# Kernel tuning notes

Measured on AMD Instinct MI355X. Metric: run time of the kernel, lower is better.

Reference implementation:

```python
import jax, jax.numpy as jnp
import numpy as np

B, S, H, D = 4, 128, 32, 128
T = 2048  # max_seq_len (cache length)
START_POS = 1024


def setup_inputs() -> dict:
    key = jax.random.key(0)
    ks = jax.random.split(key, 5)
    q = jax.random.normal(ks[0], (B, S, H, D), dtype=jnp.float32)
    k = jax.random.normal(ks[1], (B, S, H, D), dtype=jnp.float32)
    v = jax.random.normal(ks[2], (B, S, H, D), dtype=jnp.float32)
    k_cache = jax.random.normal(ks[3], (B, T, H, D), dtype=jnp.float32)
    v_cache = jax.random.normal(ks[4], (B, T, H, D), dtype=jnp.float32)
    return {"q": q, "k": k, "v": v, "k_cache": k_cache, "v_cache": v_cache,
            "input_pos": START_POS, "seq_len": S}


def reference(q, k, v, k_cache, v_cache, input_pos, seq_len):
    # Fused KV-cache append + causal SDPA (llama.sdpa_with_kv_cache semantics).
    # q/k/v: [B, S, H, D]; caches: [B, T, H, D]; input_pos = write offset.
    start = input_pos
    kc = jax.lax.dynamic_update_slice(k_cache, k, (0, start, 0, 0))
    vc = jax.lax.dynamic_update_slice(v_cache, v, (0, start, 0, 0))

    scale = 1.0 / jnp.sqrt(jnp.asarray(q.shape[-1], q.dtype))
    # scores: [B, H, S, T]
    scores = jnp.einsum('bshd,bthd->bhst', q, kc) * scale

    # causal mask relative to absolute positions: query i (global start+i)
    # attends to cache positions j <= start + i
    qpos = start + jnp.arange(seq_len)            # [S]
    kpos = jnp.arange(kc.shape[1])                # [T]
    mask = kpos[None, :] <= qpos[:, None]         # [S, T]
    neg = jnp.asarray(jnp.finfo(scores.dtype).min, scores.dtype)
    scores = jnp.where(mask[None, None], scores, neg)

    attn = jax.nn.softmax(scores, axis=-1)        # dropout = 0.0 (inference)
    out = jnp.einsum('bhst,bthd->bshd', attn, vc)  # [B, S, H, D]
    bsz = q.shape[0]
    return out.reshape(bsz, seq_len, -1)          # [B, S, H*D]
```

## Files before the change

kernel.cpp:

```cpp
#include <hip/hip_runtime.h>
#include <hip/hip_bf16.h>


typedef short bf16x8 __attribute__((ext_vector_type(8)));
typedef float f32x4  __attribute__((ext_vector_type(4)));

constexpr int B = 4, S = 128, H = 32, D = 128, T = 2048;
constexpr int QBLK = 64, KVBLK = 64;
constexpr int NS = 4;
constexpr float SCALE = 0.08838834764831845f;
constexpr float MNEG = -1e30f;

__device__ __forceinline__ short f2bf(float f) {
    return (short)__bfloat16_as_ushort(__float2bfloat16(f));
}
__device__ __forceinline__ unsigned pack_bf2(float a, float b) {
    return (unsigned)(unsigned short)__bfloat16_as_ushort(__float2bfloat16(a))
         | ((unsigned)__bfloat16_as_ushort(__float2bfloat16(b)) << 16);
}

__device__ __forceinline__ int kswz(int row, int cb) { return row * 256 + (cb ^ ((row & 7) << 4)); }
__device__ __forceinline__ int vswz(int row, int cb) { return 16384 + row * 128 + (cb ^ ((row & 7) << 4)); }

template<int MODE>
__global__ __launch_bounds__(256, 4) void sdpa_kernel(
    const float* __restrict__ qg, const float* __restrict__ kin,
    const float* __restrict__ vin, const float* __restrict__ kc,
    const float* __restrict__ vc, const int* __restrict__ ip,
    float* __restrict__ out, float* __restrict__ wsO, float2* __restrict__ wsML)
{
    __shared__ __align__(16) char smem[32768];

    const int start = ip[0];
    const int bh = blockIdx.x;
    const int b  = bh >> 5;
    const int h  = bh & 31;
    const int q0 = blockIdx.y * QBLK;
    const int z  = (MODE == 1) ? blockIdx.z : 0;
    const int t  = threadIdx.x;
    const int w  = t >> 6;
    const int l  = t & 63;
    const int l16 = l & 15;
    const int lg  = l >> 4;
    const int qi  = q0 + w * 16 + l16;

    const float* qp = qg + (((size_t)b * S + qi) * H + h) * D;
    bf16x8 qfrag[4];
    #pragma unroll
    for (int ks = 0; ks < 4; ++ks) {
        const float* p = qp + ks * 32 + lg * 8;
        #pragma unroll
        for (int i = 0; i < 8; ++i) qfrag[ks][i] = f2bf(p[i]);
    }

    f32x4 oaccT[8];
    #pragma unroll
    for (int n = 0; n < 8; ++n) oaccT[n] = {0.f, 0.f, 0.f, 0.f};
    float m = MNEG, ssum = 0.f;

    const int kv_end = start + q0 + QBLK;
    const int nt     = (kv_end + KVBLK - 1) / KVBLK;
    const int tstep  = (MODE == 1) ? NS : 1;
    const int t0     = (MODE == 1) ? z : 0;

    const int r8  = t >> 5, c = t & 31;
    const int rb  = t & 15, cb0 = t >> 4;

    auto kaddr = [&](int j) -> const float4* {
        return (j < start)
            ? (const float4*)(kc  + (((size_t)b * T + j) * H + h) * (size_t)D)
            : (const float4*)(kin + (((size_t)b * S + (j - start)) * H + h) * (size_t)D);
    };
    auto vaddr = [&](int j) -> const float4* {
        return (j < start)
            ? (const float4*)(vc  + (((size_t)b * T + j) * H + h) * (size_t)D)
            : (const float4*)(vin + (((size_t)b * S + (j - start)) * H + h) * (size_t)D);
    };

    for (int tile = t0; tile < nt; tile += tstep) {
        const int j0 = tile * KVBLK;

        #pragma unroll
        for (int g = 0; g < 2; ++g) {
            float4 kt[4];
            #pragma unroll
            for (int p = 0; p < 4; ++p) kt[p] = kaddr(j0 + (g * 4 + p) * 8 + r8)[c];
            #pragma unroll
            for (int p = 0; p < 4; ++p) {
                short4 k4b = { f2bf(kt[p].x), f2bf(kt[p].y), f2bf(kt[p].z), f2bf(kt[p].w) };
                *(short4*)(smem + kswz((g * 4 + p) * 8 + r8, c * 8)) = k4b;
            }
        }
        #pragma unroll
        for (int it = 0; it < 2; ++it) {
            const int cb = cb0 + 16 * it;
            float4 a[4];
            #pragma unroll
            for (int kk = 0; kk < 4; ++kk)
                a[kk] = vaddr(j0 + rb * 4 + kk)[cb];
            #pragma unroll
            for (int jj = 0; jj < 4; ++jj) {
                const int d = cb * 4 + jj;
                short4 wv = { f2bf(((const float*)&a[0])[jj]),
                              f2bf(((const float*)&a[1])[jj]),
                              f2bf(((const float*)&a[2])[jj]),
                              f2bf(((const float*)&a[3])[jj]) };
                *(short4*)(smem + vswz(d, rb * 8)) = wv;
            }
        }
        __syncthreads();

        f32x4 sacc[4];
        #pragma unroll
        for (int n = 0; n < 4; ++n) sacc[n] = {0.f, 0.f, 0.f, 0.f};
        #pragma unroll
        for (int n = 0; n < 4; ++n) {
            #pragma unroll
            for (int ks = 0; ks < 4; ++ks) {
                bf16x8 kfrag = *(const bf16x8*)(smem + kswz(n * 16 + l16, ks * 64 + lg * 16));
                sacc[n] = __builtin_amdgcn_mfma_f32_16x16x32_bf16(
                    kfrag, qfrag[ks], sacc[n], 0, 0, 0);
            }
        }

        float pmax = MNEG;
        #pragma unroll
        for (int n = 0; n < 4; ++n) {
            #pragma unroll
            for (int j = 0; j < 4; ++j) {
                const int kvj = j0 + n * 16 + lg * 4 + j;
                float s = sacc[n][j] * SCALE;
                if (kvj > start + qi) s = MNEG;
                sacc[n][j] = s;
                pmax = fmaxf(pmax, s);
            }
        }
        pmax = fmaxf(pmax, __shfl_xor(pmax, 16));
        pmax = fmaxf(pmax, __shfl_xor(pmax, 32));
        const float mnew = fmaxf(m, pmax);
        const float corr = __expf(m - mnew);
        m = mnew;

        float tsum = 0.f;
        unsigned plo[4], phi[4];
        #pragma unroll
        for (int n = 0; n < 4; ++n) {
            float p0 = __expf(sacc[n][0] - m);
            float p1 = __expf(sacc[n][1] - m);
            float p2 = __expf(sacc[n][2] - m);
            float p3 = __expf(sacc[n][3] - m);
            tsum += (p0 + p1) + (p2 + p3);
            plo[n] = pack_bf2(p0, p1);
            phi[n] = pack_bf2(p2, p3);
        }
        tsum += __shfl_xor(tsum, 16);
        tsum += __shfl_xor(tsum, 32);
        ssum = ssum * corr + tsum;
        #pragma unroll
        for (int n = 0; n < 8; ++n) {
            #pragma unroll
            for (int j = 0; j < 4; ++j) oaccT[n][j] *= corr;
        }

        const int sA = (((2 * lg)     & 3) << 4) | l16;
        const int sB = (((2 * lg + 1) & 3) << 4) | l16;
        const bool hi = (lg >= 2);
        bf16x8 pfragB[2];
        #pragma unroll
        for (int ks = 0; ks < 2; ++ks) {
            unsigned eA0 = __shfl(plo[2 * ks],     sA), eA1 = __shfl(phi[2 * ks],     sA);
            unsigned fA0 = __shfl(plo[2 * ks + 1], sA), fA1 = __shfl(phi[2 * ks + 1], sA);
            unsigned eB0 = __shfl(plo[2 * ks],     sB), eB1 = __shfl(phi[2 * ks],     sB);
            unsigned fB0 = __shfl(plo[2 * ks + 1], sB), fB1 = __shfl(phi[2 * ks + 1], sB);
            union { unsigned u[4]; bf16x8 v; } cv;
            cv.u[0] = hi ? fA0 : eA0;
            cv.u[1] = hi ? fA1 : eA1;
            cv.u[2] = hi ? fB0 : eB0;
            cv.u[3] = hi ? fB1 : eB1;
            pfragB[ks] = cv.v;
        }

        #pragma unroll
        for (int ks = 0; ks < 2; ++ks) {
            #pragma unroll
            for (int n = 0; n < 8; ++n) {
                bf16x8 vfrag = *(const bf16x8*)(smem + vswz(n * 16 + l16, ks * 64 + lg * 16));
                oaccT[n] = __builtin_amdgcn_mfma_f32_16x16x32_bf16(
                    vfrag, pfragB[ks], oaccT[n], 0, 0, 0);
            }
        }
        __syncthreads();
    }

    float* scr = (float*)(smem + w * 8192);
    const float inv = (MODE == 0) ? 1.0f / ssum : 1.0f;
    #pragma unroll
    for (int n = 0; n < 8; ++n) {
        #pragma unroll
        for (int j = 0; j < 4; ++j) {
            const int d = n * 16 + lg * 4 + j;
            scr[l16 * 128 + (d ^ ((l16 & 7) << 2))] = oaccT[n][j] * inv;
        }
    }
    asm volatile("s_waitcnt lgkmcnt(0)" ::: "memory");
    __builtin_amdgcn_sched_barrier(0);
    #pragma unroll
    for (int cc = 0; cc < 8; ++cc) {
        const int r  = cc * 2 + (l >> 5);
        const int dw = (l & 31) * 4;
        f32x4 val = *(f32x4*)&scr[r * 128 + (dw ^ ((r & 7) << 2))];
        const int qr = q0 + w * 16 + r;
        if (MODE == 0) {
            *(f32x4*)(out + ((size_t)b * S + qr) * (size_t)(H * D) + h * D + dw) = val;
        } else {
            *(f32x4*)(wsO + ((((size_t)z * B + b) * S + qr) * H + h) * (size_t)D + dw) = val;
        }
    }
    if (MODE == 1 && lg == 0)
        wsML[(((size_t)z * B + b) * S + qi) * H + h] = make_float2(m, ssum);
}

__global__ __launch_bounds__(256) void combine_kernel(
    const float* __restrict__ wsO, const float2* __restrict__ wsML,
    float* __restrict__ out)
{
    constexpr int R    = B * S * H;
    constexpr int TOT4 = R * D / 4;
    for (int i4 = blockIdx.x * 256 + threadIdx.x; i4 < TOT4;
         i4 += gridDim.x * 256) {
        const int row = i4 >> 5;
        float2 e[NS];
        float M = MNEG;
        #pragma unroll
        for (int cc = 0; cc < NS; ++cc) {
            e[cc] = wsML[(size_t)cc * R + row];
            M = fmaxf(M, e[cc].x);
        }
        float L = 0.f;
        float v0 = 0.f, v1 = 0.f, v2 = 0.f, v3 = 0.f;
        #pragma unroll
        for (int cc = 0; cc < NS; ++cc) {
            const float wgt = __expf(e[cc].x - M);
            L += e[cc].y * wgt;
            float4 tv = ((const float4*)wsO)[(size_t)cc * TOT4 + i4];
            v0 += tv.x * wgt; v1 += tv.y * wgt; v2 += tv.z * wgt; v3 += tv.w * wgt;
        }
        const float inv = 1.0f / L;
        ((float4*)out)[i4] = make_float4(v0 * inv, v1 * inv, v2 * inv, v3 * inv);
    }
}

extern "C" void kernel_launch(void* const* d_in, const int* in_sizes, int n_in,
                              void* d_out, int out_size, void* d_ws, size_t ws_size,
                              hipStream_t stream) {
    const float* q  = (const float*)d_in[0];
    const float* k  = (const float*)d_in[1];
    const float* v  = (const float*)d_in[2];
    const float* kc = (const float*)d_in[3];
    const float* vc = (const float*)d_in[4];
    const int*   ip = (const int*)d_in[5];
    float* out = (float*)d_out;

    const size_t nO  = (size_t)NS * B * S * H * D;
    const size_t nML = (size_t)NS * B * S * H;
    const size_t need = (nO + 2 * nML) * sizeof(float);

    if (ws_size >= need) {
        float*  wsO  = (float*)d_ws;
        float2* wsML = (float2*)(wsO + nO);
        sdpa_kernel<1><<<dim3(B * H, S / QBLK, NS), 256, 0, stream>>>(
            q, k, v, kc, vc, ip, out, wsO, wsML);
        combine_kernel<<<2048, 256, 0, stream>>>(wsO, wsML, out);
    } else {
        sdpa_kernel<0><<<dim3(B * H, S / QBLK), 256, 0, stream>>>(
            q, k, v, kc, vc, ip, out, nullptr, nullptr);
    }
}
```

Measured before the change: 50.38 us.

## Process all 128 queries per block with 8 warps to share KV tiles

Each block now covers the full query length (S=128) using 512 threads and 8 waves instead of two 64-query blocks, so every K/V tile is loaded from global memory and converted to bf16 once rather than twice. Waves whose query rows are fully masked for a tile skip the compute, and the output epilogue is split into two halves to fit the per-wave scratch within the existing shared memory. The cost is half as many blocks in the grid, which lowers parallelism, plus more threads sharing each barrier.

Result: faster. 45.48 us (median of 4 runs) (-9.7%).

```diff
diff --git a/kernel.cpp b/kernel.cpp
--- a/kernel.cpp
+++ b/kernel.cpp
@@ -6,7 +6,7 @@
 typedef float f32x4  __attribute__((ext_vector_type(4)));
 
 constexpr int B = 4, S = 128, H = 32, D = 128, T = 2048;
-constexpr int QBLK = 64, KVBLK = 64;
+constexpr int KVBLK = 64;
 constexpr int NS = 4;
 constexpr float SCALE = 0.08838834764831845f;
 constexpr float MNEG = -1e30f;
@@ -23,7 +23,7 @@
 __device__ __forceinline__ int vswz(int row, int cb) { return 16384 + row * 128 + (cb ^ ((row & 7) << 4)); }
 
 template<int MODE>
-__global__ __launch_bounds__(256, 4) void sdpa_kernel(
+__global__ __launch_bounds__(512, 2) void sdpa_kernel(
     const float* __restrict__ qg, const float* __restrict__ kin,
     const float* __restrict__ vin, const float* __restrict__ kc,
     const float* __restrict__ vc, const int* __restrict__ ip,
@@ -35,14 +35,13 @@
     const int bh = blockIdx.x;
     const int b  = bh >> 5;
     const int h  = bh & 31;
-    const int q0 = blockIdx.y * QBLK;
     const int z  = (MODE == 1) ? blockIdx.z : 0;
     const int t  = threadIdx.x;
     const int w  = t >> 6;
     const int l  = t & 63;
     const int l16 = l & 15;
     const int lg  = l >> 4;
-    const int qi  = q0 + w * 16 + l16;
+    const int qi  = w * 16 + l16;
 
     const float* qp = qg + (((size_t)b * S + qi) * H + h) * D;
     bf16x8 qfrag[4];
@@ -58,13 +57,13 @@
     for (int n = 0; n < 8; ++n) oaccT[n] = {0.f, 0.f, 0.f, 0.f};
     float m = MNEG, ssum = 0.f;
 
-    const int kv_end = start + q0 + QBLK;
+    const int kv_end = start + S;
     const int nt     = (kv_end + KVBLK - 1) / KVBLK;
     const int tstep  = (MODE == 1) ? NS : 1;
     const int t0     = (MODE == 1) ? z : 0;
 
-    const int r8  = t >> 5, c = t & 31;
-    const int rb  = t & 15, cb0 = t >> 4;
+    const int kr = t >> 5, c = t & 31;
+    const int rb = t & 15, cb = t >> 4;
 
     auto kaddr = [&](int j) -> const float4* {
         return (j < start)
@@ -82,18 +81,16 @@
 
         #pragma unroll
         for (int g = 0; g < 2; ++g) {
-            float4 kt[4];
-            #pragma unroll
-            for (int p = 0; p < 4; ++p) kt[p] = kaddr(j0 + (g * 4 + p) * 8 + r8)[c];
-            #pragma unroll
-            for (int p = 0; p < 4; ++p) {
+            float4 kt[2];
+            #pragma unroll
+            for (int p = 0; p < 2; ++p) kt[p] = kaddr(j0 + (g * 2 + p) * 16 + kr)[c];
+            #pragma unroll
+            for (int p = 0; p < 2; ++p) {
                 short4 k4b = { f2bf(kt[p].x), f2bf(kt[p].y), f2bf(kt[p].z), f2bf(kt[p].w) };
-                *(short4*)(smem + kswz((g * 4 + p) * 8 + r8, c * 8)) = k4b;
-            }
-        }
-        #pragma unroll
-        for (int it = 0; it < 2; ++it) {
-            const int cb = cb0 + 16 * it;
+                *(short4*)(smem + kswz((g * 2 + p) * 16 + kr, c * 8)) = k4b;
+            }
+        }
+        {
             float4 a[4];
             #pragma unroll
             for (int kk = 0; kk < 4; ++kk)
@@ -110,111 +107,121 @@
         }
         __syncthreads();
 
-        f32x4 sacc[4];
-        #pragma unroll
-        for (int n = 0; n < 4; ++n) sacc[n] = {0.f, 0.f, 0.f, 0.f};
-        #pragma unroll
-        for (int n = 0; n < 4; ++n) {
-            #pragma unroll
-            for (int ks = 0; ks < 4; ++ks) {
-                bf16x8 kfrag = *(const bf16x8*)(smem + kswz(n * 16 + l16, ks * 64 + lg * 16));
-                sacc[n] = __builtin_amdgcn_mfma_f32_16x16x32_bf16(
-                    kfrag, qfrag[ks], sacc[n], 0, 0, 0);
-            }
-        }
-
-        float pmax = MNEG;
-        #pragma unroll
-        for (int n = 0; n < 4; ++n) {
-            #pragma unroll
-            for (int j = 0; j < 4; ++j) {
-                const int kvj = j0 + n * 16 + lg * 4 + j;
-                float s = sacc[n][j] * SCALE;
-                if (kvj > start + qi) s = MNEG;
-                sacc[n][j] = s;
-                pmax = fmaxf(pmax, s);
-            }
-        }
-        pmax = fmaxf(pmax, __shfl_xor(pmax, 16));
-        pmax = fmaxf(pmax, __shfl_xor(pmax, 32));
-        const float mnew = fmaxf(m, pmax);
-        const float corr = __expf(m - mnew);
-        m = mnew;
-
-        float tsum = 0.f;
-        unsigned plo[4], phi[4];
-        #pragma unroll
-        for (int n = 0; n < 4; ++n) {
-            float p0 = __expf(sacc[n][0] - m);
-            float p1 = __expf(sacc[n][1] - m);
-            float p2 = __expf(sacc[n][2] - m);
-            float p3 = __expf(sacc[n][3] - m);
-            tsum += (p0 + p1) + (p2 + p3);
-            plo[n] = pack_bf2(p0, p1);
-            phi[n] = pack_bf2(p2, p3);
-        }
-        tsum += __shfl_xor(tsum, 16);
-        tsum += __shfl_xor(tsum, 32);
-        ssum = ssum * corr + tsum;
-        #pragma unroll
-        for (int n = 0; n < 8; ++n) {
-            #pragma unroll
-            for (int j = 0; j < 4; ++j) oaccT[n][j] *= corr;
-        }
-
-        const int sA = (((2 * lg)     & 3) << 4) | l16;
-        const int sB = (((2 * lg + 1) & 3) << 4) | l16;
-        const bool hi = (lg >= 2);
-        bf16x8 pfragB[2];
-        #pragma unroll
-        for (int ks = 0; ks < 2; ++ks) {
-            unsigned eA0 = __shfl(plo[2 * ks],     sA), eA1 = __shfl(phi[2 * ks],     sA);
-            unsigned fA0 = __shfl(plo[2 * ks + 1], sA), fA1 = __shfl(phi[2 * ks + 1], sA);
-            unsigned eB0 = __shfl(plo[2 * ks],     sB), eB1 = __shfl(phi[2 * ks],     sB);
-            unsigned fB0 = __shfl(plo[2 * ks + 1], sB), fB1 = __shfl(phi[2 * ks + 1], sB);
-            union { unsigned u[4]; bf16x8 v; } cv;
-            cv.u[0] = hi ? fA0 : eA0;
-            cv.u[1] = hi ? fA1 : eA1;
-            cv.u[2] = hi ? fB0 : eB0;
-            cv.u[3] = hi ? fB1 : eB1;
-            pfragB[ks] = cv.v;
-        }
-
-        #pragma unroll
-        for (int ks = 0; ks < 2; ++ks) {
+        if (j0 <= start + w * 16 + 15) {
+            f32x4 sacc[4];
+            #pragma unroll
+            for (int n = 0; n < 4; ++n) sacc[n] = {0.f, 0.f, 0.f, 0.f};
+            #pragma unroll
+            for (int n = 0; n < 4; ++n) {
+                #pragma unroll
+                for (int ks = 0; ks < 4; ++ks) {
+                    bf16x8 kfrag = *(const bf16x8*)(smem + kswz(n * 16 + l16, ks * 64 + lg * 16));
+                    sacc[n] = __builtin_amdgcn_mfma_f32_16x16x32_bf16(
+                        kfrag, qfrag[ks], sacc[n], 0, 0, 0);
+                }
+            }
+
+            float pmax = MNEG;
+            #pragma unroll
+            for (int n = 0; n < 4; ++n) {
+                #pragma unroll
+                for (int j = 0; j < 4; ++j) {
+                    const int kvj = j0 + n * 16 + lg * 4 + j;
+                    float s = sacc[n][j] * SCALE;
+                    if (kvj > start + qi) s = MNEG;
+                    sacc[n][j] = s;
+                    pmax = fmaxf(pmax, s);
+                }
+            }
+            pmax = fmaxf(pmax, __shfl_xor(pmax, 16));
+            pmax = fmaxf(pmax, __shfl_xor(pmax, 32));
+            const float mnew = fmaxf(m, pmax);
+            const float corr = __expf(m - mnew);
+            m = mnew;
+
+            float tsum = 0.f;
+            unsigned plo[4], phi[4];
+            #pragma unroll
+            for (int n = 0; n < 4; ++n) {
+                float p0 = __expf(sacc[n][0] - m);
+                float p1 = __expf(sacc[n][1] - m);
+                float p2 = __expf(sacc[n][2] - m);
+                float p3 = __expf(sacc[n][3] - m);
+                tsum += (p0 + p1) + (p2 + p3);
+                plo[n] = pack_bf2(p0, p1);
+                phi[n] = pack_bf2(p2, p3);
+            }
+            tsum += __shfl_xor(tsum, 16);
+            tsum += __shfl_xor(tsum, 32);
+            ssum = ssum * corr + tsum;
             #pragma unroll
             for (int n = 0; n < 8; ++n) {
-                bf16x8 vfrag = *(const bf16x8*)(smem + vswz(n * 16 + l16, ks * 64 + lg * 16));
-                oaccT[n] = __builtin_amdgcn_mfma_f32_16x16x32_bf16(
-                    vfrag, pfragB[ks], oaccT[n], 0, 0, 0);
+                #pragma unroll
+                for (int j = 0; j < 4; ++j) oaccT[n][j] *= corr;
+            }
+
+            const int sA = (((2 * lg)     & 3) << 4) | l16;
+            const int sB = (((2 * lg + 1) & 3) << 4) | l16;
+            const bool hi = (lg >= 2);
+            bf16x8 pfragB[2];
+            #pragma unroll
+            for (int ks = 0; ks < 2; ++ks) {
+                unsigned eA0 = __shfl(plo[2 * ks],     sA), eA1 = __shfl(phi[2 * ks],     sA);
+                unsigned fA0 = __shfl(plo[2 * ks + 1], sA), fA1 = __shfl(phi[2 * ks + 1], sA);
+                unsigned eB0 = __shfl(plo[2 * ks],     sB), eB1 = __shfl(phi[2 * ks],     sB);
+                unsigned fB0 = __shfl(plo[2 * ks + 1], sB), fB1 = __shfl(phi[2 * ks + 1], sB);
+                union { unsigned u[4]; bf16x8 v; } cv;
+                cv.u[0] = hi ? fA0 : eA0;
+                cv.u[1] = hi ? fA1 : eA1;
+                cv.u[2] = hi ? fB0 : eB0;
+                cv.u[3] = hi ? fB1 : eB1;
+                pfragB[ks] = cv.v;
+            }
+
+            #pragma unroll
+            for (int ks = 0; ks < 2; ++ks) {
+                #pragma unroll
+                for (int n = 0; n < 8; ++n) {
+                    bf16x8 vfrag = *(const bf16x8*)(smem + vswz(n * 16 + l16, ks * 64 + lg * 16));
+                    oaccT[n] = __builtin_amdgcn_mfma_f32_16x16x32_bf16(
+                        vfrag, pfragB[ks], oaccT[n], 0, 0, 0);
+                }
             }
         }
         __syncthreads();
     }
 
-    float* scr = (float*)(smem + w * 8192);
+    float* scr = (float*)(smem + w * 4096);
     const float inv = (MODE == 0) ? 1.0f / ssum : 1.0f;
     #pragma unroll
-    for (int n = 0; n < 8; ++n) {
-        #pragma unroll
-        for (int j = 0; j < 4; ++j) {
-            const int d = n * 16 + lg * 4 + j;
-            scr[l16 * 128 + (d ^ ((l16 & 7) << 2))] = oaccT[n][j] * inv;
-        }
-    }
-    asm volatile("s_waitcnt lgkmcnt(0)" ::: "memory");
-    __builtin_amdgcn_sched_barrier(0);
-    #pragma unroll
-    for (int cc = 0; cc < 8; ++cc) {
-        const int r  = cc * 2 + (l >> 5);
-        const int dw = (l & 31) * 4;
-        f32x4 val = *(f32x4*)&scr[r * 128 + (dw ^ ((r & 7) << 2))];
-        const int qr = q0 + w * 16 + r;
-        if (MODE == 0) {
-            *(f32x4*)(out + ((size_t)b * S + qr) * (size_t)(H * D) + h * D + dw) = val;
-        } else {
-            *(f32x4*)(wsO + ((((size_t)z * B + b) * S + qr) * H + h) * (size_t)D + dw) = val;
-        }
+    for (int half = 0; half < 2; ++half) {
+        #pragma unroll
+        for (int n2 = 0; n2 < 4; ++n2) {
+            const int n = half * 4 + n2;
+            #pragma unroll
+            for (int j = 0; j < 4; ++j) {
+                const int dl = n2 * 16 + lg * 4 + j;
+                scr[l16 * 64 + (((dl & ~3) ^ ((l16 & 7) << 2)) | (dl & 3))] =
+                    oaccT[n][j] * inv;
+            }
+        }
+        asm volatile("s_waitcnt lgkmcnt(0)" ::: "memory");
+        __builtin_amdgcn_sched_barrier(0);
+        #pragma unroll
+        for (int pass = 0; pass < 4; ++pass) {
+            const int r  = pass * 4 + (l >> 4);
+            const int d0 = (l & 15) * 4;
+            f32x4 val = *(f32x4*)&scr[r * 64 + (d0 ^ ((r & 7) << 2))];
+            const int qr = w * 16 + r;
+            const int dc = half * 64 + d0;
+            if (MODE == 0) {
+                *(f32x4*)(out + ((size_t)b * S + qr) * (size_t)(H * D) + h * D + dc) = val;
+            } else {
+                *(f32x4*)(wsO + ((((size_t)z * B + b) * S + qr) * H + h) * (size_t)D + dc) = val;
+            }
+        }
+        asm volatile("s_waitcnt lgkmcnt(0)" ::: "memory");
+        __builtin_amdgcn_sched_barrier(0);
     }
     if (MODE == 1 && lg == 0)
         wsML[(((size_t)z * B + b) * S + qi) * H + h] = make_float2(m, ssum);
@@ -268,11 +275,11 @@
     if (ws_size >= need) {
         float*  wsO  = (float*)d_ws;
         float2* wsML = (float2*)(wsO + nO);
-        sdpa_kernel<1><<<dim3(B * H, S / QBLK, NS), 256, 0, stream>>>(
+        sdpa_kernel<1><<<dim3(B * H, 1, NS), 512, 0, stream>>>(
             q, k, v, kc, vc, ip, out, wsO, wsML);
         combine_kernel<<<2048, 256, 0, stream>>>(wsO, wsML, out);
     } else {
-        sdpa_kernel<0><<<dim3(B * H, S / QBLK), 256, 0, stream>>>(
+        sdpa_kernel<0><<<dim3(B * H), 512, 0, stream>>>(
             q, k, v, kc, vc, ip, out, nullptr, nullptr);
     }
 }
```
